# Optimization experiments

Hardware: AMD Instinct MI355X
Metric: run time of the kernel (lower is better)

## Reference

```python
import jax, jax.numpy as jnp
import numpy as np

# Model dims (rexgen/WLN canonical hyperparameters)
B, N, MAXNB, NBONDS = 16, 100, 10, 120
AF, BF, H, BIN = 82, 6, 300, 11
DEPTH, K = 3, 80


def setup_inputs() -> dict:
    key = jax.random.key(0)
    ks = jax.random.split(key, 24)
    f32 = jnp.float32
    inp = {}
    inp["fatoms"] = jax.random.normal(ks[0], (B, N, AF), f32)
    inp["fbonds"] = jax.random.normal(ks[1], (B, NBONDS, BF), f32)
    inp["atom_nb"] = jax.random.randint(ks[2], (B, N, MAXNB), 0, N)
    inp["bond_nb"] = jax.random.randint(ks[3], (B, N, MAXNB), 0, NBONDS)
    inp["num_nbs"] = jnp.full((B, N), MAXNB, jnp.int32)
    inp["n_atoms"] = jnp.full((B,), N, jnp.int32)
    inp["binary_feats"] = jax.random.normal(ks[4], (B, N, N, BIN), f32)
    inp["mask_neis"] = (jax.random.uniform(ks[5], (B, N, MAXNB, 1)) > 0.2).astype(f32)
    inp["mask_atoms"] = jnp.ones((B, N, 1), f32)
    # sparse_idx enumerates all (sample, atom_i, atom_j) pairs in row-major order
    sb = jnp.repeat(jnp.arange(B), N * N)
    si = jnp.tile(jnp.repeat(jnp.arange(N), N), B)
    sj = jnp.tile(jnp.arange(N), B * N)
    inp["sparse_idx"] = jnp.stack([sb, si, sj], axis=1).astype(jnp.int32)

    def w(k, shape):
        return jax.random.normal(k, shape, f32) * 0.1

    # WLNet params
    inp["W_atom"] = w(ks[6], (AF, H))
    inp["W_nei_atom"] = w(ks[7], (H, H))
    inp["W_nei_bond"] = w(ks[8], (BF, H))
    inp["W_self"] = w(ks[9], (H, H))
    inp["W_U2"] = w(ks[10], (H + BF, H)); inp["b_U2"] = jnp.zeros((H,), f32)
    inp["W_U1"] = w(ks[11], (2 * H, H)); inp["b_U1"] = jnp.zeros((H,), f32)
    # Attention params
    inp["W_att_local"] = w(ks[12], (H, H))
    inp["W_att_bin"] = w(ks[13], (BIN, H)); inp["b_att"] = jnp.zeros((H,), f32)
    inp["W_att_score"] = w(ks[14], (H, 1)); inp["b_att_score"] = jnp.zeros((1,), f32)
    # ReactivityScoring params
    inp["W_pl"] = w(ks[15], (H, H))
    inp["W_pg"] = w(ks[16], (H, H))
    inp["W_pb"] = w(ks[17], (BIN, H)); inp["b_p"] = jnp.zeros((H,), f32)
    inp["W_out"] = w(ks[18], (H, 1)); inp["b_out"] = jnp.zeros((1,), f32)
    return inp


def _pair_scores(fatoms, fbonds, binary_feats, mask_neis, mask_atoms,
                 W_atom, W_nei_atom, W_nei_bond, W_self, W_U2, b_U2, W_U1, b_U1,
                 W_att_local, W_att_bin, b_att, W_att_score, b_att_score,
                 W_pl, W_pg, W_pb, b_p, W_out, b_out,
                 atom_nb, bond_nb, sparse_idx):
    bidx = jnp.arange(B)[:, None, None]
    # --- WLNet graph convolution ---
    h = jax.nn.relu(fatoms @ W_atom)                       # [B,N,H]
    local = h
    for _ in range(DEPTH):
        fnei_atom = h[bidx, atom_nb]                       # [B,N,MAXNB,H]
        fnei_bond = fbonds[bidx, bond_nb]                  # [B,N,MAXNB,BF]
        h_nei = (fnei_atom @ W_nei_atom) * (fnei_bond @ W_nei_bond)
        f_nei = (h_nei * mask_neis).sum(axis=2)            # [B,N,H]
        f_self = h @ W_self
        local = f_nei * f_self * mask_atoms                # kernel output
        nei_label = jax.nn.relu(jnp.concatenate([fnei_atom, fnei_bond], -1) @ W_U2 + b_U2)
        nei_label = (nei_label * mask_neis).sum(axis=2)
        h = jax.nn.relu(jnp.concatenate([h, nei_label], -1) @ W_U1 + b_U1)
    # --- Global attention over atom pairs ---
    pair = local[:, :, None, :] + local[:, None, :, :]     # [B,N,N,H]
    att_h = jax.nn.relu(pair @ W_att_local + binary_feats @ W_att_bin + b_att)
    att_s = jax.nn.sigmoid(att_h @ W_att_score + b_att_score)  # [B,N,N,1]
    ctx = jnp.einsum('bij,bjh->bih', att_s[..., 0], local)     # [B,N,H]
    # --- Gather sparse pairs and score reactivity ---
    sb, si, sj = sparse_idx[:, 0], sparse_idx[:, 1], sparse_idx[:, 2]
    local_pair = local[sb, si] + local[sb, sj]             # [P,H]
    global_pair = ctx[sb, si] + ctx[sb, sj]                # [P,H]
    bin_pair = binary_feats[sb, si, sj]                    # [P,BIN]
    hid = jax.nn.relu(local_pair @ W_pl + global_pair @ W_pg + bin_pair @ W_pb + b_p)
    return hid @ W_out + b_out                             # [P,1]


def reference(fatoms, fbonds, atom_nb, bond_nb, num_nbs, n_atoms, binary_feats,
              mask_neis, mask_atoms, sparse_idx,
              W_atom, W_nei_atom, W_nei_bond, W_self, W_U2, b_U2, W_U1, b_U1,
              W_att_local, W_att_bin, b_att, W_att_score, b_att_score,
              W_pl, W_pg, W_pb, b_p, W_out, b_out):
    pair_scores = _pair_scores(fatoms, fbonds, binary_feats, mask_neis, mask_atoms,
                               W_atom, W_nei_atom, W_nei_bond, W_self, W_U2, b_U2, W_U1, b_U1,
                               W_att_local, W_att_bin, b_att, W_att_score, b_att_score,
                               W_pl, W_pg, W_pb, b_p, W_out, b_out,
                               atom_nb, bond_nb, sparse_idx)
    # Segmented top-k: sparse_idx rows are grouped & ordered by sample with
    # exactly N*N pairs each, so per-sample flatten == reshape to [B, N*N].
    _, topks = jax.lax.top_k(pair_scores.reshape(B, N * N), K)  # indices, matching torch.topk[1]
    return pair_scores, topks
```

## Files before the change

### kernel.cpp

```cpp
#include <hip/hip_runtime.h>
#include <hip/hip_bf16.h>
#include <math.h>

#define BB 16
#define NN 100
#define MAXNB 10
#define NBONDS 120
#define AF 82
#define BF 6
#define HH 300
#define BIN 11
#define DEPTH 3
#define KTOP 80

typedef __attribute__((ext_vector_type(8))) short short8;
typedef __attribute__((ext_vector_type(4))) float floatx4;

__device__ __forceinline__ unsigned short f2bf(float f) {
    unsigned int u = __float_as_uint(f);
    unsigned int r = (u + 0x7FFFu + ((u >> 16) & 1u)) >> 16;
    return (unsigned short)r;
}
__device__ __forceinline__ float bf2f(unsigned short h) {
    return __uint_as_float(((unsigned int)h) << 16);
}

#define O_WATOM 0
#define O_WNB   29184
#define O_U2B   38912
#define O_WNA   48640
#define O_P1    145920
#define O_P2    243200
#define O_U1CAT 340480
#define O_WATT  535040
#define O_WPL   632320
#define O_WPG   729600

__global__ __launch_bounds__(256) void k_prep(
    const float* __restrict__ s0, const float* __restrict__ s1,
    const float* __restrict__ s2, const float* __restrict__ s3,
    const float* __restrict__ s4, const float* __restrict__ s5,
    const float* __restrict__ s6, const float* __restrict__ s7,
    const float* __restrict__ s8, const float* __restrict__ s9,
    const float* __restrict__ s10,
    unsigned short* __restrict__ WTh, unsigned short* __restrict__ WTl,
    const float* __restrict__ fatoms, const float* __restrict__ fbonds,
    unsigned short* __restrict__ fatomsbf, unsigned short* __restrict__ fbondsbf,
    const float* __restrict__ bin, unsigned short* __restrict__ BINBF,
    const float* __restrict__ Wbin0, const float* __restrict__ Wbin1,
    unsigned short* __restrict__ WBF0, unsigned short* __restrict__ WBF1)
{
    const int z = blockIdx.z;
    if (z == 11) {
        int idx = blockIdx.x * 256 + threadIdx.x;
        if (idx < 1600 * 96) {
            int r = idx / 96, c = idx - r * 96;
            float f = (c < AF) ? fatoms[r * AF + c] : 0.f;
            unsigned short hb = f2bf(f);
            fatomsbf[r * 192 + c]      = hb;
            fatomsbf[r * 192 + 96 + c] = f2bf(f - bf2f(hb));
        } else {
            int i2 = idx - 1600 * 96;
            if (i2 < 1920 * 32) {
                int r = i2 / 32, c = i2 - r * 32;
                float f = (c < BF) ? fbonds[r * BF + c] : 0.f;
                unsigned short hb = f2bf(f);
                fbondsbf[r * 64 + c]      = hb;
                fbondsbf[r * 64 + 32 + c] = f2bf(f - bf2f(hb));
            }
        }
        return;
    }
    if (z == 12) {
        const int bx = blockIdx.x;
        if (bx < 625) {
            int p = bx * 256 + threadIdx.x;
            if (p < BB * NN * NN) {
                const float* src = bin + (size_t)p * BIN;
                unsigned short tmp[16];
#pragma unroll
                for (int k = 0; k < BIN; k++) tmp[k] = f2bf(src[k]);
#pragma unroll
                for (int k = BIN; k < 16; k++) tmp[k] = 0;
                *(uint4*)(BINBF + (size_t)p * 16) = *(uint4*)tmp;
                *(uint4*)(BINBF + (size_t)p * 16 + 8) = *(uint4*)(tmp + 8);
            }
        } else if (bx < 663) {
            int zb = bx - 625;
            const float* src = (zb >= 19) ? Wbin1 : Wbin0;
            unsigned short* dst = (zb >= 19) ? WBF1 : WBF0;
            int idx = (zb % 19) * 256 + threadIdx.x;
            int jj = idx & 7;
            int koct = (idx >> 3) & 1;
            int n = (idx >> 4) & 15;
            int ch = idx >> 8;
            int k = koct * 8 + jj;
            int h = ch * 16 + n;
            float f = (k < BIN && h < 300) ? src[k * 300 + h] : 0.f;
            dst[idx] = f2bf(f);
        }
        return;
    }
    const float* src; int K, kc, off, u1base = -1;
    switch (z) {
        case 0:  src = s0;  K = AF;  kc = 3;  off = O_WATOM; break;
        case 1:  src = s1;  K = BF;  kc = 1;  off = O_WNB;   break;
        case 2:  src = s2;  K = BF;  kc = 1;  off = O_U2B;   break;
        case 3:  src = s3;  K = HH;  kc = 10; off = O_WNA;   break;
        case 4:  src = s4;  K = HH;  kc = 10; off = O_P1;    break;
        case 5:  src = s5;  K = HH;  kc = 10; off = O_P2;    break;
        case 6:  src = s6;  K = HH;  kc = 10; off = O_U1CAT; u1base = 0;  break;
        case 7:  src = s7;  K = HH;  kc = 10; off = O_U1CAT; u1base = 10; break;
        case 8:  src = s8;  K = HH;  kc = 10; off = O_WATT;  break;
        case 9:  src = s9;  K = HH;  kc = 10; off = O_WPL;   break;
        default: src = s10; K = HH;  kc = 10; off = O_WPG;   break;
    }
    const int lim = 9728 * kc;
    int i = blockIdx.x * 256 + threadIdx.x;
    if (i < lim) {
        int jj = i & 7;
        int lane = (i >> 3) & 63;
        int rem = i >> 9;
        int kci = rem % kc;
        int ct = rem / kc;
        int k = kci * 32 + (lane >> 4) * 8 + jj;
        int col = ct * 16 + (lane & 15);
        float f = (k < K && col < 300) ? src[k * 300 + col] : 0.f;
        unsigned short hb = f2bf(f);
        int dsti = (u1base >= 0)
                 ? off + ct * 10240 + (kci + u1base) * 512 + lane * 8 + jj
                 : off + i;
        WTh[dsti] = hb;
        WTl[dsti] = f2bf(f - bf2f(hb));
    }
}

__device__ __forceinline__ void gemm_core(
    const unsigned short* __restrict__ A, int lda, int kc, int M,
    const unsigned short* __restrict__ wthB, const unsigned short* __restrict__ wtlB,
    float* __restrict__ C, int ldc,
    const float* __restrict__ bias,
    const float* __restrict__ Add, int ldAdd, int addOff,
    int act, unsigned short* __restrict__ Cbf,
    int row0, int gcolBase)
{
    __shared__ unsigned short sa[16 * 648];
    if (row0 >= M) return;
    const int tid = threadIdx.x;
    const int lane = tid & 63;
    const int wid = tid >> 6;
    const int sR = kc * 64 + 8;

    {
        const uint4* Ag = (const uint4*)A;
        uint4* sa4 = (uint4*)sa;
        const int q4 = kc * 8;
        const int lda4 = lda >> 3;
        const int sR4 = q4 + 1;
        for (int i = tid; i < 16 * q4; i += 256) {
            int r = i / q4, q = i - r * q4;
            sa4[r * sR4 + q] = Ag[(size_t)(row0 + r) * lda4 + q];
        }
    }
    __syncthreads();

    const int ct = blockIdx.y * 4 + wid;
    if (ct >= 19) return;

    const int m = lane & 15;
    const int rq = lane >> 4;
    const int koct8 = rq * 8;
    const unsigned short* wth = wthB + (size_t)ct * kc * 512;
    const unsigned short* wtl = wtlB + (size_t)ct * kc * 512;

    floatx4 acc = {0.f, 0.f, 0.f, 0.f};
    for (int kci = 0; kci < kc; kci++) {
        short8 ah = *(const short8*)(sa + m * sR + kci * 32 + koct8);
        short8 al = *(const short8*)(sa + m * sR + kc * 32 + kci * 32 + koct8);
        short8 wh = *(const short8*)(wth + (kci * 64 + lane) * 8);
        short8 wl = *(const short8*)(wtl + (kci * 64 + lane) * 8);
        acc = __builtin_amdgcn_mfma_f32_16x16x32_bf16(ah, wl, acc, 0, 0, 0);
        acc = __builtin_amdgcn_mfma_f32_16x16x32_bf16(al, wh, acc, 0, 0, 0);
        acc = __builtin_amdgcn_mfma_f32_16x16x32_bf16(ah, wh, acc, 0, 0, 0);
    }

    const int col = ct * 16 + m;
    if (col < 300) {
        const float bv = bias ? bias[col] : 0.f;
        const int gcol = gcolBase + col;
#pragma unroll
        for (int r = 0; r < 4; r++) {
            const int grow = row0 + rq * 4 + r;
            float v = acc[r] + bv;
            if (Add) v += Add[(size_t)grow * ldAdd + addOff + col];
            if (act) v = fmaxf(v, 0.f);
            if (C) C[(size_t)grow * ldc + gcol] = v;
            if (Cbf) {
                unsigned short hb = f2bf(v);
                Cbf[(size_t)grow * 640 + col]       = hb;
                Cbf[(size_t)grow * 640 + 320 + col] = f2bf(v - bf2f(hb));
            }
        }
    }
}

__global__ __launch_bounds__(256) void k_gemm_mfma(
    const unsigned short* __restrict__ A, int lda, int kc, int M,
    const unsigned short* __restrict__ WTh, const unsigned short* __restrict__ WTl,
    int wtStride,
    float* __restrict__ C, int ldc,
    const float* __restrict__ bias,
    const float* __restrict__ Add, int ldAdd, int addOff,
    int act, unsigned short* __restrict__ Cbf)
{
    const int widx = blockIdx.z;
    gemm_core(A, lda, kc, M,
              WTh + (size_t)widx * wtStride, WTl + (size_t)widx * wtStride,
              C, ldc, bias, Add, ldAdd, addOff, act, Cbf,
              blockIdx.x * 16, widx * 300);
}

__global__ __launch_bounds__(256) void k_gemm_u1(
    const unsigned short* __restrict__ Ah,
    const unsigned short* __restrict__ An,
    const unsigned short* __restrict__ WTh, const unsigned short* __restrict__ WTl,
    const float* __restrict__ bias,
    unsigned short* __restrict__ Cbf)
{
    __shared__ unsigned short sa[16 * 1288];
    const int row0 = blockIdx.x * 16;
    if (row0 >= 1600) return;
    const int tid = threadIdx.x;
    const int lane = tid & 63;
    const int wid = tid >> 6;

    {
        const uint4* Ag = (const uint4*)Ah;
        const uint4* Ng = (const uint4*)An;
        uint4* sa4 = (uint4*)sa;
        for (int i = tid; i < 16 * 160; i += 256) {
            int r = i / 160, q = i - r * 160;
            const size_t rb = (size_t)(row0 + r) * 80;
            uint4 v;
            if (q < 40)       v = Ag[rb + q];
            else if (q < 80)  v = Ng[rb + (q - 40)];
            else if (q < 120) v = Ag[rb + (q - 40)];
            else              v = Ng[rb + (q - 80)];
            sa4[r * 161 + q] = v;
        }
    }
    __syncthreads();

    const int ct = blockIdx.y * 4 + wid;
    if (ct >= 19) return;

    const int m = lane & 15;
    const int rq = lane >> 4;
    const int koct8 = rq * 8;
    const unsigned short* wth = WTh + (size_t)ct * 10240;
    const unsigned short* wtl = WTl + (size_t)ct * 10240;

    floatx4 acc = {0.f, 0.f, 0.f, 0.f};
    for (int kci = 0; kci < 20; kci++) {
        short8 ah = *(const short8*)(sa + m * 1288 + kci * 32 + koct8);
        short8 al = *(const short8*)(sa + m * 1288 + 640 + kci * 32 + koct8);
        short8 wh = *(const short8*)(wth + (kci * 64 + lane) * 8);
        short8 wl = *(const short8*)(wtl + (kci * 64 + lane) * 8);
        acc = __builtin_amdgcn_mfma_f32_16x16x32_bf16(ah, wl, acc, 0, 0, 0);
        acc = __builtin_amdgcn_mfma_f32_16x16x32_bf16(al, wh, acc, 0, 0, 0);
        acc = __builtin_amdgcn_mfma_f32_16x16x32_bf16(ah, wh, acc, 0, 0, 0);
    }

    const int col = ct * 16 + m;
    if (col < 300) {
        const float bv = bias[col];
#pragma unroll
        for (int r = 0; r < 4; r++) {
            const int grow = row0 + rq * 4 + r;
            float v = fmaxf(acc[r] + bv, 0.f);
            unsigned short hb = f2bf(v);
            Cbf[(size_t)grow * 640 + col]       = hb;
            Cbf[(size_t)grow * 640 + 320 + col] = f2bf(v - bf2f(hb));
        }
    }
}

__global__ __launch_bounds__(256) void k_gemm_first(
    const unsigned short* __restrict__ fatomsbf,
    const unsigned short* __restrict__ fbondsbf,
    const unsigned short* __restrict__ WTh, const unsigned short* __restrict__ WTl,
    unsigned short* __restrict__ hbf, float* __restrict__ FBout)
{
    const int z = blockIdx.z;
    if (z == 0) {
        gemm_core(fatomsbf, 192, 3, 1600,
                  WTh + O_WATOM, WTl + O_WATOM,
                  nullptr, 0, nullptr, nullptr, 0, 0, 1, hbf,
                  blockIdx.x * 16, 0);
    } else {
        const int w = z - 1;
        gemm_core(fbondsbf, 64, 1, 1920,
                  WTh + O_WNB + w * 9728, WTl + O_WNB + w * 9728,
                  FBout, 600, nullptr, nullptr, 0, 0, 0, nullptr,
                  blockIdx.x * 16, w * 300);
    }
}

__global__ __launch_bounds__(320, 4) void k_neighbor(
    const float* __restrict__ HW, const float* __restrict__ FB,
    const int* __restrict__ atom_nb, const int* __restrict__ bond_nb,
    const float* __restrict__ mask_neis, const float* __restrict__ mask_atoms,
    const float* __restrict__ b_U2,
    unsigned short* __restrict__ localbf, unsigned short* __restrict__ nlbf,
    int computeU1)
{
    __shared__ int   sAn[2][MAXNB];
    __shared__ int   sBd[2][MAXNB];
    __shared__ float sM[2][MAXNB];
    __shared__ float pF[2][300];
    __shared__ float pN[2][300];
    const int tx = threadIdx.x;
    const int ty = threadIdx.y;
    const int tz = threadIdx.z;
    const int bx = blockIdx.x;
    const int bn0 = ((bx & 15) * 50 + (bx >> 4)) * 2;
    const int flat = (tz * 2 + ty) * 80 + tx;

    if (flat < 20)       sAn[flat / 10][flat % 10] = atom_nb[(bn0 + flat / 10) * MAXNB + flat % 10];
    else if (flat < 40)  { int f = flat - 20; sBd[f / 10][f % 10] = bond_nb[(bn0 + f / 10) * MAXNB + f % 10]; }
    else if (flat < 60)  { int f = flat - 40; sM[f / 10][f % 10]  = mask_neis[(bn0 + f / 10) * MAXNB + f % 10]; }
    __syncthreads();

    const int bn = bn0 + ty;
    const int b = bn / NN;
    const int h4 = tx;
    const float4* HW4 = (const float4*)HW;
    const float4* FB4 = (const float4*)FB;

    float4 fnei = make_float4(0.f, 0.f, 0.f, 0.f);
    float4 nls  = fnei;
    if (tx < 75) {
        if (computeU1) {
            const float4 bu = ((const float4*)b_U2)[h4];
#pragma unroll
            for (int kk = 0; kk < 5; kk++) {
                const int k = tz * 5 + kk;
                const int an = sAn[ty][k];
                const int bd = sBd[ty][k];
                const float m = sM[ty][k];
                const float4* hr = HW4 + (size_t)(b * NN + an) * 225;
                const float4* fr = FB4 + (size_t)(b * NBONDS + bd) * 150;
                float4 ha = hr[h4];
                float4 hu = hr[150 + h4];
                float4 fa = fr[h4];
                float4 fu = fr[75 + h4];
                fnei.x = fmaf(m, ha.x * fa.x, fnei.x);
                fnei.y = fmaf(m, ha.y * fa.y, fnei.y);
                fnei.z = fmaf(m, ha.z * fa.z, fnei.z);
                fnei.w = fmaf(m, ha.w * fa.w, fnei.w);
                float ux = hu.x + fu.x + bu.x;
                float uy = hu.y + fu.y + bu.y;
                float uz = hu.z + fu.z + bu.z;
                float uw = hu.w + fu.w + bu.w;
                nls.x = fmaf(m, fmaxf(ux, 0.f), nls.x);
                nls.y = fmaf(m, fmaxf(uy, 0.f), nls.y);
                nls.z = fmaf(m, fmaxf(uz, 0.f), nls.z);
                nls.w = fmaf(m, fmaxf(uw, 0.f), nls.w);
            }
        } else {
#pragma unroll
            for (int kk = 0; kk < 5; kk++) {
                const int k = tz * 5 + kk;
                const int an = sAn[ty][k];
                const int bd = sBd[ty][k];
                const float m = sM[ty][k];
                float4 ha = HW4[(size_t)(b * NN + an) * 225 + h4];
                float4 fa = FB4[(size_t)(b * NBONDS + bd) * 150 + h4];
                fnei.x = fmaf(m, ha.x * fa.x, fnei.x);
                fnei.y = fmaf(m, ha.y * fa.y, fnei.y);
                fnei.z = fmaf(m, ha.z * fa.z, fnei.z);
                fnei.w = fmaf(m, ha.w * fa.w, fnei.w);
            }
        }
        if (tz == 1) {
            ((float4*)pF[ty])[h4] = fnei;
            if (computeU1) ((float4*)pN[ty])[h4] = nls;
        }
    }
    __syncthreads();

    if (tx < 75 && tz == 0) {
        const float4 pf = ((const float4*)pF[ty])[h4];
        fnei.x += pf.x; fnei.y += pf.y; fnei.z += pf.z; fnei.w += pf.w;

        const float ma = mask_atoms[bn];
        const float4 sf = HW4[(size_t)bn * 225 + 75 + h4];
        float lv[4];
        lv[0] = fnei.x * sf.x * ma; lv[1] = fnei.y * sf.y * ma;
        lv[2] = fnei.z * sf.z * ma; lv[3] = fnei.w * sf.w * ma;

        ushort4 lh, ll;
        unsigned short* lhp = (unsigned short*)&lh;
        unsigned short* llp = (unsigned short*)&ll;
#pragma unroll
        for (int c = 0; c < 4; c++) {
            unsigned short hb = f2bf(lv[c]);
            lhp[c] = hb; llp[c] = f2bf(lv[c] - bf2f(hb));
        }
        *(ushort4*)(localbf + (size_t)bn * 640 + h4 * 4)       = lh;
        *(ushort4*)(localbf + (size_t)bn * 640 + 320 + h4 * 4) = ll;

        if (computeU1) {
            const float4 pn = ((const float4*)pN[ty])[h4];
            float nv[4] = {nls.x + pn.x, nls.y + pn.y, nls.z + pn.z, nls.w + pn.w};
            ushort4 nh, nl2;
            unsigned short* nhp = (unsigned short*)&nh;
            unsigned short* nlp = (unsigned short*)&nl2;
#pragma unroll
            for (int c = 0; c < 4; c++) {
                unsigned short nb = f2bf(nv[c]);
                nhp[c] = nb; nlp[c] = f2bf(nv[c] - bf2f(nb));
            }
            *(ushort4*)(nlbf + (size_t)bn * 640 + h4 * 4)       = nh;
            *(ushort4*)(nlbf + (size_t)bn * 640 + 320 + h4 * 4) = nl2;
        }
    }
}

__global__ __launch_bounds__(256) void k_pair(
    const float* __restrict__ R, int ldr,
    const unsigned short* __restrict__ BINBF,
    const unsigned short* __restrict__ WBF,
    const float* __restrict__ bvec,
    const float* __restrict__ Wscore, const float* __restrict__ bscore,
    float* __restrict__ outp, int mode)
{
    __shared__ float sLi[16 * 308];
    __shared__ float sLj[16 * 308];

    const int b  = blockIdx.x;
    const int i0 = blockIdx.y * 16;
    const int j0 = blockIdx.z * 16;
    const int tid = threadIdx.x;
    const int lane = tid & 63;
    const int wid = tid >> 6;

    for (int idx = tid; idx < 16 * 308; idx += 256) {
        int r = idx / 308;
        int c = idx - r * 308;
        float vi = 0.f, vj = 0.f;
        if (c < 300) {
            if (i0 + r < NN) vi = R[(size_t)(b * NN + i0 + r) * ldr + c] + bvec[c];
            if (j0 + r < NN) vj = R[(size_t)(b * NN + j0 + r) * ldr + c];
        }
        sLi[idx] = vi;
        sLj[idx] = vj;
    }

    const int m = lane & 15;
    const int koct = lane >> 4;
    short8 afrag[4];
#pragma unroll
    for (int g = 0; g < 4; g++) {
        int ii = i0 + wid * 4 + g; if (ii > NN - 1) ii = NN - 1;
        int jj2 = j0 + m;          if (jj2 > NN - 1) jj2 = NN - 1;
        const size_t pidx = (size_t)((b * NN + ii) * NN + jj2);
        afrag[g] = *(const short8*)(BINBF + pidx * 16 + (koct & 1) * 8);
        if (koct >= 2) afrag[g] = short8{0,0,0,0,0,0,0,0};
    }
    __syncthreads();

    const int n = lane & 15;
    const int rquad = lane >> 4;
    const floatx4 zero = {0.f, 0.f, 0.f, 0.f};
    float su[4][4];
#pragma unroll
    for (int g = 0; g < 4; g++)
#pragma unroll
        for (int r = 0; r < 4; r++) su[g][r] = 0.f;

    for (int ch = 0; ch < 19; ch++) {
        const int h0 = ch * 16;
        short8 bfrag = {0,0,0,0,0,0,0,0};
        if (lane < 32)
            bfrag = *(const short8*)(WBF + ch * 256 + (n * 2 + koct) * 8);
        float wsv = 0.f;
        if (h0 + n < 300) wsv = Wscore[h0 + n];
#pragma unroll
        for (int g = 0; g < 4; g++) {
            floatx4 P = __builtin_amdgcn_mfma_f32_16x16x32_bf16(
                afrag[g], bfrag, zero, 0, 0, 0);
            const float liv = sLi[(wid * 4 + g) * 308 + h0 + n];
#pragma unroll
            for (int r = 0; r < 4; r++) {
                const float ljv = sLj[(rquad * 4 + r) * 308 + h0 + n];
                float u = P[r] + liv + ljv;
                su[g][r] = fmaf(fmaxf(u, 0.f), wsv, su[g][r]);
            }
        }
    }

    const float bs = bscore[0];
#pragma unroll
    for (int g = 0; g < 4; g++) {
#pragma unroll
        for (int r = 0; r < 4; r++) {
            float v = su[g][r];
            v += __shfl_xor(v, 1);
            v += __shfl_xor(v, 2);
            v += __shfl_xor(v, 4);
            v += __shfl_xor(v, 8);
            if (n == 0) {
                const int i = i0 + wid * 4 + g;
                const int j = j0 + rquad * 4 + r;
                if (i < NN && j < NN) {
                    float s = v + bs;
                    outp[(size_t)(b * NN + i) * NN + j] =
                        (mode == 0) ? (1.f / (1.f + expf(-s))) : s;
                }
            }
        }
    }
}

__global__ __launch_bounds__(320, 2) void k_ctx(
    const float* __restrict__ att, const float* __restrict__ LL,
    float* __restrict__ LPG)
{
    const int bx = blockIdx.x;
    const int b = bx & 15;
    const int i0 = (bx >> 4) * 4;
    const int tid = threadIdx.x;
    __shared__ float sa[4 * NN];
    for (int idx = tid; idx < 4 * NN; idx += 320) {
        int ii = idx / NN, j = idx - ii * NN;
        sa[idx] = att[(size_t)(b * NN + i0 + ii) * NN + j];
    }
    __syncthreads();
    if (tid < HH) {
        float acc0 = 0.f, acc1 = 0.f, acc2 = 0.f, acc3 = 0.f;
#pragma unroll 4
        for (int j = 0; j < NN; j++) {
            const float lv = LL[(size_t)(b * NN + j) * 900 + 600 + tid];
            acc0 = fmaf(sa[j], lv, acc0);
            acc1 = fmaf(sa[NN + j], lv, acc1);
            acc2 = fmaf(sa[2 * NN + j], lv, acc2);
            acc3 = fmaf(sa[3 * NN + j], lv, acc3);
        }
        float vals[4] = {acc0, acc1, acc2, acc3};
#pragma unroll
        for (int k = 0; k < 4; k++) {
            LPG[(size_t)(b * NN + i0 + k) * 300 + tid] =
                vals[k] + LL[(size_t)(b * NN + i0 + k) * 900 + 300 + tid];
        }
    }
}

__global__ __launch_bounds__(1024) void k_topk(
    const float* __restrict__ scores, float* __restrict__ topk_out)
{
    const int b = blockIdx.x;
    const int tid = threadIdx.x;
    const int wid = tid >> 6;
    const int lane = tid & 63;
    const float* sc = scores + (size_t)b * (NN * NN);

    __shared__ unsigned int skey[NN * NN];
    __shared__ unsigned int whist[16 * 256];
    __shared__ unsigned int hist[256];
    __shared__ unsigned int candU[KTOP];
    __shared__ int candI[KTOP];
    __shared__ int cntG;
    __shared__ int curMin;
    __shared__ unsigned int sh_pref, sh_mask;
    __shared__ int sh_kRem;
    __shared__ int sh_last;

    for (int idx = tid; idx < NN * NN; idx += 1024) {
        unsigned int u = __float_as_uint(sc[idx]);
        u = (u & 0x80000000u) ? ~u : (u | 0x80000000u);
        skey[idx] = u;
    }
    if (tid == 0) {
        sh_pref = 0u; sh_mask = 0u; sh_kRem = KTOP; cntG = 0; sh_last = -1;
    }
    __syncthreads();

    for (int pass = 0; pass < 4; pass++) {
        const int shift = 24 - 8 * pass;
        unsigned int* wh = whist + (wid << 8);
        wh[lane] = 0u; wh[lane + 64] = 0u; wh[lane + 128] = 0u; wh[lane + 192] = 0u;
        __syncthreads();
        const unsigned int pref = sh_pref, mask = sh_mask;
        for (int idx = tid; idx < NN * NN; idx += 1024) {
            unsigned int u = skey[idx];
            if ((u & mask) == pref)
                atomicAdd(&wh[(u >> shift) & 255u], 1u);
        }
        __syncthreads();
        if (tid < 256) {
            unsigned int s = 0u;
#pragma unroll
            for (int w = 0; w < 16; w++) s += whist[(w << 8) | tid];
            hist[tid] = s;
        }
        __syncthreads();
        if (wid == 0) {
            unsigned int h0 = hist[lane * 4 + 0];
            unsigned int h1 = hist[lane * 4 + 1];
            unsigned int h2 = hist[lane * 4 + 2];
            unsigned int h3 = hist[lane * 4 + 3];
            unsigned int own = h0 + h1 + h2 + h3;
            unsigned int suf = own;
#pragma unroll
            for (int off = 1; off < 64; off <<= 1) {
                unsigned int v = __shfl_down(suf, off);
                if (lane + off < 64) suf += v;
            }
            const int k = sh_kRem;
            const unsigned int above = suf - own;
            if (above < (unsigned int)k && suf >= (unsigned int)k) {
                unsigned int c = above, hb; int bsel;
                c += h3;
                if ((int)c >= k) { bsel = lane * 4 + 3; hb = h3; }
                else { c += h2;
                    if ((int)c >= k) { bsel = lane * 4 + 2; hb = h2; }
                    else { c += h1;
                        if ((int)c >= k) { bsel = lane * 4 + 1; hb = h1; }
                        else { c += h0; bsel = lane * 4; hb = h0; } } }
                sh_kRem = k - (int)(c - hb);
                sh_pref = pref | ((unsigned int)bsel << shift);
                sh_mask = mask | (0xFFu << shift);
            }
        }
        __syncthreads();
    }
    const unsigned int T = sh_pref;

    for (int idx = tid; idx < NN * NN; idx += 1024) {
        unsigned int u = skey[idx];
        if (u > T) {
            int pos = atomicAdd(&cntG, 1);
            candU[pos] = u;
            candI[pos] = idx;
        }
    }
    __syncthreads();
    const int needE = KTOP - cntG;

    for (int e = 0; e < needE; e++) {
        if (tid == 0) curMin = 0x7fffffff;
        __syncthreads();
        const int last = sh_last;
        for (int idx = tid; idx < NN * NN; idx += 1024) {
            if (skey[idx] == T && idx > last)
                atomicMin(&curMin, idx);
        }
        __syncthreads();
        if (tid == 0) {
            candU[cntG + e] = T;
            candI[cntG + e] = curMin;
            sh_last = curMin;
        }
        __syncthreads();
    }

    if (tid < KTOP) {
        const unsigned int mu = candU[tid];
        const int mi = candI[tid];
        int rank = 0;
        for (int o = 0; o < KTOP; o++) {
            unsigned int ou = candU[o];
            int oi = candI[o];
            if (ou > mu || (ou == mu && oi < mi)) rank++;
        }
        topk_out[b * KTOP + rank] = (float)mi;
    }
}

extern "C" void kernel_launch(void* const* d_in, const int* in_sizes, int n_in,
                              void* d_out, int out_size, void* d_ws, size_t ws_size,
                              hipStream_t stream) {
    const float* fatoms       = (const float*)d_in[0];
    const float* fbonds       = (const float*)d_in[1];
    const int*   atom_nb      = (const int*)d_in[2];
    const int*   bond_nb      = (const int*)d_in[3];
    const float* binary_feats = (const float*)d_in[6];
    const float* mask_neis    = (const float*)d_in[7];
    const float* mask_atoms   = (const float*)d_in[8];
    const float* W_atom       = (const float*)d_in[10];
    const float* W_nei_atom   = (const float*)d_in[11];
    const float* W_nei_bond   = (const float*)d_in[12];
    const float* W_self       = (const float*)d_in[13];
    const float* W_U2         = (const float*)d_in[14];
    const float* b_U2         = (const float*)d_in[15];
    const float* W_U1         = (const float*)d_in[16];
    const float* b_U1         = (const float*)d_in[17];
    const float* W_att_local  = (const float*)d_in[18];
    const float* W_att_bin    = (const float*)d_in[19];
    const float* b_att        = (const float*)d_in[20];
    const float* W_att_score  = (const float*)d_in[21];
    const float* b_att_score  = (const float*)d_in[22];
    const float* W_pl         = (const float*)d_in[23];
    const float* W_pg         = (const float*)d_in[24];
    const float* W_pb         = (const float*)d_in[25];
    const float* b_p          = (const float*)d_in[26];
    const float* W_out        = (const float*)d_in[27];
    const float* b_out        = (const float*)d_in[28];

    float* ws = (float*)d_ws;
    float* HW  = ws;
    float* FB  = HW + 1440000;
    float* LL  = FB + 1152000;
    float* LPG = LL + 1440000;
    float* att = LPG + 480000;
    unsigned short* S0       = (unsigned short*)(ws + 4672000);
    unsigned short* hbf      = S0;
    unsigned short* hbf2     = S0 + 1024000;
    unsigned short* nlbf     = S0 + 2048000;
    unsigned short* localbf  = S0 + 3072000;
    unsigned short* WTh      = S0 + 4096000;
    unsigned short* WTl      = S0 + 4922880;
    unsigned short* BINBF    = S0 + 5749760;
    unsigned short* WBF_att  = S0 + 8309760;
    unsigned short* WBF_fin  = S0 + 8314624;
    unsigned short* fatomsbf = S0 + 8319488;
    unsigned short* fbondsbf = S0 + 8626688;

    float* out = (float*)d_out;
    float* topk_out = out + (size_t)BB * NN * NN;

    k_prep<<<dim3(840, 1, 13), 256, 0, stream>>>(
        W_atom, W_nei_bond, W_U2 + 300 * 300, W_nei_atom, W_self, W_U2,
        W_U1, W_U1 + 300 * 300, W_att_local, W_pl, W_pg, WTh, WTl,
        fatoms, fbonds, fatomsbf, fbondsbf,
        binary_feats, BINBF, W_att_bin, W_pb, WBF_att, WBF_fin);

    k_gemm_first<<<dim3(120, 5, 3), 256, 0, stream>>>(
        fatomsbf, fbondsbf, WTh, WTl, hbf, FB);

    unsigned short* hb[2] = {hbf, hbf2};
    int cur = 0;
    for (int d = 0; d < DEPTH; d++) {
        int nW = (d == DEPTH - 1) ? 2 : 3;
        k_gemm_mfma<<<dim3(104, 5, nW), 256, 0, stream>>>(
            hb[cur], 640, 10, 1600, WTh + O_WNA, WTl + O_WNA, 97280,
            HW, 900, nullptr, nullptr, 0, 0, 0, nullptr);
        k_neighbor<<<dim3(800), dim3(80, 2, 2), 0, stream>>>(
            HW, FB, atom_nb, bond_nb, mask_neis, mask_atoms, b_U2,
            localbf, nlbf, (d < DEPTH - 1) ? 1 : 0);
        if (d < DEPTH - 1) {
            k_gemm_u1<<<dim3(104, 5, 1), 256, 0, stream>>>(
                hb[cur], nlbf, WTh + O_U1CAT, WTl + O_U1CAT, b_U1, hb[cur ^ 1]);
            cur ^= 1;
        }
    }

    k_gemm_mfma<<<dim3(104, 5, 3), 256, 0, stream>>>(
        localbf, 640, 10, 1600, WTh + O_WATT, WTl + O_WATT, 97280,
        LL, 900, nullptr, nullptr, 0, 0, 0, nullptr);

    k_pair<<<dim3(16, 7, 7), 256, 0, stream>>>(
        LL, 900, BINBF, WBF_att, b_att, W_att_score, b_att_score,
        att, 0);

    k_ctx<<<dim3(BB * 25), 320, 0, stream>>>(att, LL, LPG);

    k_pair<<<dim3(16, 7, 7), 256, 0, stream>>>(
        LPG, 300, BINBF, WBF_fin, b_p, W_out, b_out,
        out, 1);

    k_topk<<<dim3(BB), 1024, 0, stream>>>(out, topk_out);
}
```

Measured before the change: 283.8 us.

## Flatten prep grid, trim GEMM epilogue args, and early-exit radix top-k

Result: no change. 284.8 us, median of 2 (+0.3%).

```diff
diff --git a/kernel.cpp b/kernel.cpp
--- a/kernel.cpp
+++ b/kernel.cpp
@@ -50,9 +50,17 @@
     const float* __restrict__ Wbin0, const float* __restrict__ Wbin1,
     unsigned short* __restrict__ WBF0, unsigned short* __restrict__ WBF1)
 {
-    const int z = blockIdx.z;
+    const int bx0 = blockIdx.x;
+    int z, bxl;
+    if (bx0 < 114)       { z = 0;  bxl = bx0; }
+    else if (bx0 < 152)  { z = 1;  bxl = bx0 - 114; }
+    else if (bx0 < 190)  { z = 2;  bxl = bx0 - 152; }
+    else if (bx0 < 3230) { int t = bx0 - 190; z = 3 + t / 380; bxl = t % 380; }
+    else if (bx0 < 4070) { z = 11; bxl = bx0 - 3230; }
+    else                 { z = 12; bxl = bx0 - 4070; }
+
     if (z == 11) {
-        int idx = blockIdx.x * 256 + threadIdx.x;
+        int idx = bxl * 256 + threadIdx.x;
         if (idx < 1600 * 96) {
             int r = idx / 96, c = idx - r * 96;
             float f = (c < AF) ? fatoms[r * AF + c] : 0.f;
@@ -72,9 +80,8 @@
         return;
     }
     if (z == 12) {
-        const int bx = blockIdx.x;
-        if (bx < 625) {
-            int p = bx * 256 + threadIdx.x;
+        if (bxl < 625) {
+            int p = bxl * 256 + threadIdx.x;
             if (p < BB * NN * NN) {
                 const float* src = bin + (size_t)p * BIN;
                 unsigned short tmp[16];
@@ -85,8 +92,8 @@
                 *(uint4*)(BINBF + (size_t)p * 16) = *(uint4*)tmp;
                 *(uint4*)(BINBF + (size_t)p * 16 + 8) = *(uint4*)(tmp + 8);
             }
-        } else if (bx < 663) {
-            int zb = bx - 625;
+        } else if (bxl < 663) {
+            int zb = bxl - 625;
             const float* src = (zb >= 19) ? Wbin1 : Wbin0;
             unsigned short* dst = (zb >= 19) ? WBF1 : WBF0;
             int idx = (zb % 19) * 256 + threadIdx.x;
@@ -116,7 +123,7 @@
         default: src = s10; K = HH;  kc = 10; off = O_WPG;   break;
     }
     const int lim = 9728 * kc;
-    int i = blockIdx.x * 256 + threadIdx.x;
+    int i = bxl * 256 + threadIdx.x;
     if (i < lim) {
         int jj = i & 7;
         int lane = (i >> 3) & 63;
@@ -140,7 +147,6 @@
     const unsigned short* __restrict__ wthB, const unsigned short* __restrict__ wtlB,
     float* __restrict__ C, int ldc,
     const float* __restrict__ bias,
-    const float* __restrict__ Add, int ldAdd, int addOff,
     int act, unsigned short* __restrict__ Cbf,
     int row0, int gcolBase)
 {
@@ -192,7 +198,6 @@
         for (int r = 0; r < 4; r++) {
             const int grow = row0 + rq * 4 + r;
             float v = acc[r] + bv;
-            if (Add) v += Add[(size_t)grow * ldAdd + addOff + col];
             if (act) v = fmaxf(v, 0.f);
             if (C) C[(size_t)grow * ldc + gcol] = v;
             if (Cbf) {
@@ -210,13 +215,12 @@
     int wtStride,
     float* __restrict__ C, int ldc,
     const float* __restrict__ bias,
-    const float* __restrict__ Add, int ldAdd, int addOff,
     int act, unsigned short* __restrict__ Cbf)
 {
     const int widx = blockIdx.z;
     gemm_core(A, lda, kc, M,
               WTh + (size_t)widx * wtStride, WTl + (size_t)widx * wtStride,
-              C, ldc, bias, Add, ldAdd, addOff, act, Cbf,
+              C, ldc, bias, act, Cbf,
               blockIdx.x * 16, widx * 300);
 }
 
@@ -295,13 +299,13 @@
     if (z == 0) {
         gemm_core(fatomsbf, 192, 3, 1600,
                   WTh + O_WATOM, WTl + O_WATOM,
-                  nullptr, 0, nullptr, nullptr, 0, 0, 1, hbf,
+                  nullptr, 0, nullptr, 1, hbf,
                   blockIdx.x * 16, 0);
     } else {
         const int w = z - 1;
         gemm_core(fbondsbf, 64, 1, 1920,
                   WTh + O_WNB + w * 9728, WTl + O_WNB + w * 9728,
-                  FBout, 600, nullptr, nullptr, 0, 0, 0, nullptr,
+                  FBout, 600, nullptr, 0, nullptr,
                   blockIdx.x * 16, w * 300);
     }
 }
@@ -556,6 +560,7 @@
     }
 }
 
+#define TCAP 512
 __global__ __launch_bounds__(1024) void k_topk(
     const float* __restrict__ scores, float* __restrict__ topk_out)
 {
@@ -568,13 +573,14 @@
     __shared__ unsigned int skey[NN * NN];
     __shared__ unsigned int whist[16 * 256];
     __shared__ unsigned int hist[256];
-    __shared__ unsigned int candU[KTOP];
-    __shared__ int candI[KTOP];
+    __shared__ unsigned int candU[TCAP];
+    __shared__ int candI[TCAP];
     __shared__ int cntG;
     __shared__ int curMin;
     __shared__ unsigned int sh_pref, sh_mask;
     __shared__ int sh_kRem;
     __shared__ int sh_last;
+    __shared__ int sh_hb;
 
     for (int idx = tid; idx < NN * NN; idx += 1024) {
         unsigned int u = __float_as_uint(sc[idx]);
@@ -583,6 +589,7 @@
     }
     if (tid == 0) {
         sh_pref = 0u; sh_mask = 0u; sh_kRem = KTOP; cntG = 0; sh_last = -1;
+        sh_hb = 0x7fffffff;
     }
     __syncthreads();
 
@@ -631,9 +638,11 @@
                 sh_kRem = k - (int)(c - hb);
                 sh_pref = pref | ((unsigned int)bsel << shift);
                 sh_mask = mask | (0xFFu << shift);
+                sh_hb = (int)hb;
             }
         }
         __syncthreads();
+        if (sh_hb <= TCAP - KTOP) break;
     }
     const unsigned int T = sh_pref;
 
@@ -641,12 +650,12 @@
         unsigned int u = skey[idx];
         if (u > T) {
             int pos = atomicAdd(&cntG, 1);
-            candU[pos] = u;
-            candI[pos] = idx;
+            if (pos < TCAP) { candU[pos] = u; candI[pos] = idx; }
         }
     }
     __syncthreads();
-    const int needE = KTOP - cntG;
+    const int cg = (cntG < TCAP) ? cntG : TCAP;
+    const int needE = KTOP - cg;
 
     for (int e = 0; e < needE; e++) {
         if (tid == 0) curMin = 0x7fffffff;
@@ -658,23 +667,25 @@
         }
         __syncthreads();
         if (tid == 0) {
-            candU[cntG + e] = T;
-            candI[cntG + e] = curMin;
+            candU[cg + e] = T;
+            candI[cg + e] = curMin;
             sh_last = curMin;
         }
         __syncthreads();
     }
 
-    if (tid < KTOP) {
+    const int nc = (cg < KTOP) ? KTOP : cg;
+    if (tid < nc) {
         const unsigned int mu = candU[tid];
         const int mi = candI[tid];
         int rank = 0;
-        for (int o = 0; o < KTOP; o++) {
+        for (int o = 0; o < nc; o++) {
             unsigned int ou = candU[o];
             int oi = candI[o];
             if (ou > mu || (ou == mu && oi < mi)) rank++;
         }
-        topk_out[b * KTOP + rank] = (float)mi;
+        if (rank < KTOP)
+            topk_out[b * KTOP + rank] = (float)mi;
     }
 }
 
@@ -730,7 +741,7 @@
     float* out = (float*)d_out;
     float* topk_out = out + (size_t)BB * NN * NN;
 
-    k_prep<<<dim3(840, 1, 13), 256, 0, stream>>>(
+    k_prep<<<dim3(4733), 256, 0, stream>>>(
         W_atom, W_nei_bond, W_U2 + 300 * 300, W_nei_atom, W_self, W_U2,
         W_U1, W_U1 + 300 * 300, W_att_local, W_pl, W_pg, WTh, WTl,
         fatoms, fbonds, fatomsbf, fbondsbf,
@@ -745,12 +756,12 @@
         int nW = (d == DEPTH - 1) ? 2 : 3;
         k_gemm_mfma<<<dim3(104, 5, nW), 256, 0, stream>>>(
             hb[cur], 640, 10, 1600, WTh + O_WNA, WTl + O_WNA, 97280,
-            HW, 900, nullptr, nullptr, 0, 0, 0, nullptr);
+            HW, 900, nullptr, 0, nullptr);
         k_neighbor<<<dim3(800), dim3(80, 2, 2), 0, stream>>>(
             HW, FB, atom_nb, bond_nb, mask_neis, mask_atoms, b_U2,
             localbf, nlbf, (d < DEPTH - 1) ? 1 : 0);
         if (d < DEPTH - 1) {
-            k_gemm_u1<<<dim3(104, 5, 1), 256, 0, stream>>>(
+            k_gemm_u1<<<dim3(100, 5, 1), 256, 0, stream>>>(
                 hb[cur], nlbf, WTh + O_U1CAT, WTl + O_U1CAT, b_U1, hb[cur ^ 1]);
             cur ^= 1;
         }
@@ -758,7 +769,7 @@
 
     k_gemm_mfma<<<dim3(104, 5, 3), 256, 0, stream>>>(
         localbf, 640, 10, 1600, WTh + O_WATT, WTl + O_WATT, 97280,
-        LL, 900, nullptr, nullptr, 0, 0, 0, nullptr);
+        LL, 900, nullptr, 0, nullptr);
 
     k_pair<<<dim3(16, 7, 7), 256, 0, stream>>>(
         LL, 900, BINBF, WBF_att, b_att, W_att_score, b_att_score,
```
